# Kernel optimization log

Hardware: AMD Instinct MI355X
Metric: run time of the kernel (lower is better)

The kernel has to match this reference:

```python
import jax, jax.numpy as jnp
import numpy as np

H = 128; D = 16; L = 4
NP_ = 50000; NL_ = 10000; EPP = 500000; ELP = 100000; EPL = 100000


def _rbf(d):
    # GaussianSmearing(start=0, stop=8, num_gaussians=16)
    off = jnp.linspace(0.0, 8.0, D)
    coeff = -0.5 / ((8.0 / (D - 1)) ** 2)
    x = d[:, None] - off[None, :]
    return jnp.exp(coeff * x * x)


def _layer_norm(x, w, b, eps=1e-5):
    mu = jnp.mean(x, axis=-1, keepdims=True)
    var = jnp.var(x, axis=-1, keepdims=True)
    return (x - mu) * jax.lax.rsqrt(var + eps) * w + b


def _block(x_src, x_dst, src, dst, ea, Wf_, bf_, Ws_, bs_, bnw, bnb, lnw, lnb):
    # CGConv message: z = [x_i(dst), x_j(src), edge_attr]
    z = jnp.concatenate([x_dst[dst], x_src[src], ea], axis=-1)  # [E, 2H+D]
    m = jax.nn.sigmoid(z @ Wf_ + bf_) * jax.nn.softplus(z @ Ws_ + bs_)
    agg = jax.ops.segment_sum(m, dst, num_segments=x_dst.shape[0])
    # BatchNorm1d in eval mode with running_mean=0, running_var=1
    agg = agg * (bnw / jnp.sqrt(1.0 + 1e-5)) + bnb
    out = agg + x_dst            # CGConv internal residual
    out = _layer_norm(out, lnw, lnb)
    out = jax.nn.relu(out)
    return out + x_dst           # ResidualCGConvBlock residual (dropout=identity in eval)


def setup_inputs() -> dict:
    key = jax.random.key(0)
    ks = jax.random.split(key, 16)
    s = lambda n: 1.0 / np.sqrt(n)
    inp = {
        'x_protein': jax.random.normal(ks[0], (NP_, 6), jnp.float32),
        'x_ligand': jax.random.normal(ks[1], (NL_, 6), jnp.float32),
        'ei_pp': jnp.stack([jax.random.randint(ks[2], (EPP,), 0, NP_),
                            jax.random.randint(ks[3], (EPP,), 0, NP_)]).astype(jnp.int32),
        'ea_pp': jax.random.uniform(ks[4], (EPP,), jnp.float32, 0.0, 8.0),
        'ei_lp': jnp.stack([jax.random.randint(ks[5], (ELP,), 0, NL_),
                            jax.random.randint(ks[6], (ELP,), 0, NP_)]).astype(jnp.int32),
        'ea_lp': jax.random.uniform(ks[7], (ELP,), jnp.float32, 0.0, 8.0),
        'ei_pl': jnp.stack([jax.random.randint(ks[8], (EPL,), 0, NP_),
                            jax.random.randint(ks[9], (EPL,), 0, NL_)]).astype(jnp.int32),
        'ea_pl': jax.random.uniform(ks[10], (EPL,), jnp.float32, 0.0, 8.0),
        'Wp': jax.random.normal(ks[11], (6, H), jnp.float32) * s(6),
        'bp': jnp.zeros((H,), jnp.float32),
        'Wl': jax.random.normal(ks[12], (6, H), jnp.float32) * s(6),
        'bl': jnp.zeros((H,), jnp.float32),
        'Wf': jax.random.normal(ks[13], (L, 3, 2 * H + D, H), jnp.float32) * s(2 * H + D),
        'bf': jnp.zeros((L, 3, H), jnp.float32),
        'Ws': jax.random.normal(ks[14], (L, 3, 2 * H + D, H), jnp.float32) * s(2 * H + D),
        'bs': jnp.zeros((L, 3, H), jnp.float32),
        'bn_w': jnp.ones((L, 3, H), jnp.float32),
        'bn_b': jnp.zeros((L, 3, H), jnp.float32),
        'ln_w': jnp.ones((L, 3, H), jnp.float32),
        'ln_b': jnp.zeros((L, 3, H), jnp.float32),
        'lno_w': jnp.ones((H,), jnp.float32),
        'lno_b': jnp.zeros((H,), jnp.float32),
        'fc_w': jax.random.normal(ks[15], (H, 21), jnp.float32) * s(H),
        'fc_b': jnp.zeros((21,), jnp.float32),
    }
    return inp


def reference(x_protein, x_ligand, ei_pp, ea_pp, ei_lp, ea_lp, ei_pl, ea_pl,
              Wp, bp, Wl, bl, Wf, bf, Ws, bs, bn_w, bn_b, ln_w, ln_b,
              lno_w, lno_b, fc_w, fc_b):
    xp = x_protein @ Wp + bp
    xl = x_ligand @ Wl + bl
    rpp = _rbf(ea_pp); rlp = _rbf(ea_lp); rpl = _rbf(ea_pl)
    for l in range(L):
        # HeteroConv aggr='sum': protein receives from pp and lp; ligand from pl
        p_pp = _block(xp, xp, ei_pp[0], ei_pp[1], rpp, Wf[l, 0], bf[l, 0], Ws[l, 0], bs[l, 0],
                      bn_w[l, 0], bn_b[l, 0], ln_w[l, 0], ln_b[l, 0])
        p_lp = _block(xl, xp, ei_lp[0], ei_lp[1], rlp, Wf[l, 1], bf[l, 1], Ws[l, 1], bs[l, 1],
                      bn_w[l, 1], bn_b[l, 1], ln_w[l, 1], ln_b[l, 1])
        l_pl = _block(xp, xl, ei_pl[0], ei_pl[1], rpl, Wf[l, 2], bf[l, 2], Ws[l, 2], bs[l, 2],
                      bn_w[l, 2], bn_b[l, 2], ln_w[l, 2], ln_b[l, 2])
        xp, xl = p_pp + p_lp, l_pl
    out = _layer_norm(xp, lno_w, lno_b)
    return out @ fc_w + fc_b
```

## Files before the change

kernel.cpp:

```cpp
#include <hip/hip_runtime.h>
#include <hip/hip_bf16.h>
#include <math.h>

#define H 128
#define LOG2E 1.44269504f

typedef _Float16 f16;
typedef _Float16 f16x2 __attribute__((ext_vector_type(2)));
typedef _Float16 f16x8 __attribute__((ext_vector_type(8)));
typedef float f32x4 __attribute__((ext_vector_type(4)));
typedef float f32x2 __attribute__((ext_vector_type(2)));
typedef unsigned int uint32;

union u2h { uint32 u; f16x2 h; };
static __device__ __forceinline__ f16x2 as_h2(uint32 v){ u2h x; x.u = v; return x.h; }
static __device__ __forceinline__ uint32 pack_h2(float a, float b){
  u2h p; p.h = (f16x2){(f16)a, (f16)b}; return p.u;
}

static __device__ __forceinline__ int unperm64(int r){
  int base = r & ~63; int g = r & 63; int t = g >> 4; int j = g & 15;
  return base + 4*j + t;
}

#define NBIN 256
#define PREP_WP_N (4*1024*128)
#define PREP_WL_N (4*512*128)
#define RBF_N     (12*(NBIN+1)*128)

__global__ void prep_all(const float* __restrict__ Wf, const float* __restrict__ Ws,
                         const float* __restrict__ bfv, const float* __restrict__ bsv,
                         f16* __restrict__ Wt_p, float* __restrict__ Bias_p,
                         f16* __restrict__ Wt_l, float* __restrict__ Bias_l,
                         f16* __restrict__ T2,
                         const float* __restrict__ Xp, const float* __restrict__ Wp,
                         const float* __restrict__ bp, f16* __restrict__ Xph, int NP,
                         const float* __restrict__ Xl, const float* __restrict__ Wl,
                         const float* __restrict__ bl, f16* __restrict__ Xlh, int NL){
  int t = blockIdx.x*blockDim.x + threadIdx.x;
  if (t < PREP_WP_N){
    int k = t & 127; int idx = t >> 7;
    int rs = idx & 1023; int l = idx >> 10;
    int r = unperm64(rs);
    int rel, c, row0; const float* W; float bias = 0.f;
    if (r < 512){
      rel = (r < 256) ? 0 : 2;
      int rr = r & 255; int j = rr & 3;
      W = (j >= 2) ? Ws : Wf;
      c = ((rr >> 2) << 1) | (j & 1);
      row0 = 128;
    }
    else if (r < 640) { rel=0; c=r-512; row0=0; W=Wf; bias = bfv[(l*3+rel)*H+c]; }
    else if (r < 768) { rel=0; c=r-640; row0=0; W=Ws; bias = bsv[(l*3+rel)*H+c]; }
    else if (r < 896) { rel=1; c=r-768; row0=0; W=Wf; bias = bfv[(l*3+rel)*H+c]; }
    else              { rel=1; c=r-896; row0=0; W=Ws; bias = bsv[(l*3+rel)*H+c]; }
    Wt_p[t] = (f16)(LOG2E * W[((size_t)(l*3+rel)*272 + row0 + k)*H + c]);
    if (k == 0) Bias_p[l*1024 + r] = LOG2E * bias;
    return;
  }
  t -= PREP_WP_N;
  if (t < PREP_WL_N){
    int k = t & 127; int idx = t >> 7;
    int rs = idx & 511; int l = idx >> 9;
    int r = unperm64(rs);
    int rel, c, row0; const float* W; float bias = 0.f;
    if (r < 256){
      rel = 1; int j = r & 3;
      W = (j >= 2) ? Ws : Wf;
      c = ((r >> 2) << 1) | (j & 1);
      row0 = 128;
    }
    else if (r < 384) { rel=2; c=r-256; row0=0; W=Wf; bias = bfv[(l*3+rel)*H+c]; }
    else              { rel=2; c=r-384; row0=0; W=Ws; bias = bsv[(l*3+rel)*H+c]; }
    Wt_l[t] = (f16)(LOG2E * W[((size_t)(l*3+rel)*272 + row0 + k)*H + c]);
    if (k == 0) Bias_l[l*512 + r] = LOG2E * bias;
    return;
  }
  t -= PREP_WL_N;
  if (t < RBF_N){
    int c = t & 127;
    int b = (t >> 7) % (NBIN+1);
    int pr = t / ((NBIN+1)*128);
    float d0 = (float)b * (8.0f/(float)NBIN);
    const float* wf = Wf + ((size_t)pr*272 + 256)*H + c;
    const float* ws = Ws + ((size_t)pr*272 + 256)*H + c;
    float f0=0.f, s0=0.f;
    #pragma unroll
    for (int k=0;k<16;k++){
      float o = 0.533333333f*(float)k;
      float tt = d0 - o;
      float r0 = __expf(-1.7578125f*tt*tt);
      f0 += r0*wf[(size_t)k*H]; s0 += r0*ws[(size_t)k*H];
    }
    f16* o = T2 + ((size_t)(pr*(NBIN+1) + b))*256;
    int m = c >> 1, sub = c & 1;
    o[4*m + sub]     = (f16)(LOG2E * f0);
    o[4*m + 2 + sub] = (f16)(LOG2E * s0);
    return;
  }
  t -= RBF_N;
  {
    int idx = t;
    const float* Xin; const float* W; const float* b; f16* Xh;
    if (idx < NP*H){ Xin=Xp; W=Wp; b=bp; Xh=Xph; }
    else { idx -= NP*H; if (idx >= NL*H) return; Xin=Xl; W=Wl; b=bl; Xh=Xlh; }
    int n = idx >> 7, c = idx & 127;
    float acc = b[c];
    #pragma unroll
    for (int k=0;k<6;k++) acc += Xin[n*6+k] * W[k*H+c];
    Xh[idx] = (f16)acc;
  }
}

__global__ void hist3_k(const int* __restrict__ dpp, int Epp,
                        const int* __restrict__ dlp, int Elp,
                        const int* __restrict__ dpl, int Epl,
                        int* __restrict__ cpp, int* __restrict__ clp, int* __restrict__ cpl){
  int e = blockIdx.x*blockDim.x + threadIdx.x;
  if (e < Epp) atomicAdd(&cpp[dpp[e]], 1);
  else if (e < Epp+Elp) atomicAdd(&clp[dlp[e-Epp]], 1);
  else if (e < Epp+Elp+Epl) atomicAdd(&cpl[dpl[e-Epp-Elp]], 1);
}

#define SCH 1024

__global__ void __launch_bounds__(256) chunksum_k(
    const int* __restrict__ counts, int NP, int NL, int Cpp, int Cpl,
    int* __restrict__ chsum){
  __shared__ int wred[4];
  int b = blockIdx.x;
  const int* cnt; int n; int ch;
  if (b < Cpp){ cnt = counts; n = NP; ch = b; }
  else if (b < 2*Cpp){ cnt = counts + NP; n = NP; ch = b - Cpp; }
  else { cnt = counts + 2*NP; n = NL; ch = b - 2*Cpp; }
  int base = ch * SCH;
  int tid = threadIdx.x;
  int s = 0;
  #pragma unroll
  for (int j=0;j<SCH/256;j++){
    int i = base + tid + j*256;
    if (i < n) s += cnt[i];
  }
  #pragma unroll
  for (int o=32;o>=1;o>>=1) s += __shfl_xor(s,o,64);
  if ((tid & 63) == 0) wred[tid>>6] = s;
  __syncthreads();
  if (tid == 0) chsum[b] = wred[0]+wred[1]+wred[2]+wred[3];
}

__global__ void __launch_bounds__(192) scanmid_k(
    int* __restrict__ chsum, int Cpp, int Cpl, int NP, int NL,
    int* __restrict__ rp_pp, int* __restrict__ rp_lp, int* __restrict__ rp_pl){
  int wid = threadIdx.x >> 6, lane = threadIdx.x & 63;
  int C, off; int* rp_end; int n;
  if (wid == 0){ C = Cpp; off = 0;      rp_end = rp_pp; n = NP; }
  else if (wid == 1){ C = Cpp; off = Cpp; rp_end = rp_lp; n = NP; }
  else { C = Cpl; off = 2*Cpp; rp_end = rp_pl; n = NL; }
  int v = (lane < C) ? chsum[off + lane] : 0;
  int x = v;
  #pragma unroll
  for (int o=1;o<64;o<<=1){
    int y = __shfl_up(x, o, 64);
    if (lane >= o) x += y;
  }
  if (lane < C) chsum[off + lane] = x - v;
  if (lane == 63) rp_end[n] = x;
}

__global__ void __launch_bounds__(1024) scanfin_k(
    const int* __restrict__ counts, int NP, int NL, int Cpp, int Cpl,
    const int* __restrict__ chsum,
    int* __restrict__ rp_pp, int* __restrict__ cur_pp,
    int* __restrict__ rp_lp, int* __restrict__ cur_lp,
    int* __restrict__ rp_pl, int* __restrict__ cur_pl){
  __shared__ int wsum[16];
  int b = blockIdx.x;
  const int* cnt; int n, ch; int* rp; int* cur;
  if (b < Cpp){ cnt = counts; n = NP; ch = b; rp = rp_pp; cur = cur_pp; }
  else if (b < 2*Cpp){ cnt = counts + NP; n = NP; ch = b - Cpp; rp = rp_lp; cur = cur_lp; }
  else { cnt = counts + 2*NP; n = NL; ch = b - 2*Cpp; rp = rp_pl; cur = cur_pl; }
  int tid = threadIdx.x, lane = tid & 63, wid = tid >> 6;
  int i = ch*SCH + tid;
  int v = (i < n) ? cnt[i] : 0;
  int x = v;
  #pragma unroll
  for (int o=1;o<64;o<<=1){
    int y = __shfl_up(x, o, 64);
    if (lane >= o) x += y;
  }
  if (lane == 63) wsum[wid] = x;
  __syncthreads();
  if (wid == 0 && lane < 16){
    int w = wsum[lane];
    #pragma unroll
    for (int o=1;o<16;o<<=1){
      int y = __shfl_up(w, o, 64);
      if (lane >= o) w += y;
    }
    wsum[lane] = w;
  }
  __syncthreads();
  int waveoff = (wid == 0) ? 0 : wsum[wid-1];
  int ex = chsum[b] + waveoff + x - v;
  if (i < n){ rp[i] = ex; cur[i] = ex; }
}

__global__ void fill3_k(const int* __restrict__ ei_pp, const float* __restrict__ ea_pp, int Epp,
                        const int* __restrict__ ei_lp, const float* __restrict__ ea_lp, int Elp,
                        const int* __restrict__ ei_pl, const float* __restrict__ ea_pl, int Epl,
                        int* __restrict__ cur_pp, int2* __restrict__ e2_pp,
                        int* __restrict__ cur_lp, int2* __restrict__ e2_lp,
                        int* __restrict__ cur_pl, int2* __restrict__ e2_pl){
  int e = blockIdx.x*blockDim.x + threadIdx.x;
  if (e < Epp){
    int p = atomicAdd(&cur_pp[ei_pp[Epp + e]], 1);
    e2_pp[p] = make_int2(ei_pp[e], __float_as_int(ea_pp[e]));
  } else if (e < Epp+Elp){
    int i = e - Epp;
    int p = atomicAdd(&cur_lp[ei_lp[Elp + i]], 1);
    e2_lp[p] = make_int2(ei_lp[i], __float_as_int(ea_lp[i]));
  } else if (e < Epp+Elp+Epl){
    int i = e - Epp - Elp;
    int p = atomicAdd(&cur_pl[ei_pl[Epl + i]], 1);
    e2_pl[p] = make_int2(ei_pl[i], __float_as_int(ea_pl[i]));
  }
}

__global__ void __launch_bounds__(256) degbin_hist(
    const int* __restrict__ rp_pp, const int* __restrict__ rp_lp,
    const int* __restrict__ rp_pl, int NP, int NL, int* __restrict__ hist){
  __shared__ int lh[128];
  int t = threadIdx.x;
  if (t < 128) lh[t] = 0;
  __syncthreads();
  int i = blockIdx.x*256 + t;
  if (i < NP){
    int d = (rp_pp[i+1]-rp_pp[i]) + (rp_lp[i+1]-rp_lp[i]);
    if (d > 63) d = 63;
    atomicAdd(&lh[63 - d], 1);
  } else if (i < NP+NL){
    int n = i - NP;
    int d = rp_pl[n+1]-rp_pl[n];
    if (d > 63) d = 63;
    atomicAdd(&lh[64 + 63 - d], 1);
  }
  __syncthreads();
  if (t < 128 && lh[t]) atomicAdd(&hist[t], lh[t]);
}

__global__ void __launch_bounds__(128) degbin_scan(
    const int* __restrict__ hist, int* __restrict__ cursor){
  int t = threadIdx.x, lane = t & 63;
  int v = hist[t];
  int x = v;
  #pragma unroll
  for (int o=1;o<64;o<<=1){
    int y = __shfl_up(x, o, 64);
    if (lane >= o) x += y;
  }
  cursor[t] = x - v;
}

__global__ void __launch_bounds__(256) degbin_scatter(
    const int* __restrict__ rp_pp, const int* __restrict__ rp_lp,
    const int* __restrict__ rp_pl, int NP, int NL,
    int* __restrict__ cursor, int* __restrict__ perm){
  __shared__ int lh[128], lbase[128], lrank[128];
  int t = threadIdx.x;
  if (t < 128){ lh[t] = 0; lrank[t] = 0; }
  __syncthreads();
  int i = blockIdx.x*256 + t;
  int bin = -1, n = 0;
  if (i < NP){
    n = i;
    int d = (rp_pp[i+1]-rp_pp[i]) + (rp_lp[i+1]-rp_lp[i]);
    if (d > 63) d = 63;
    bin = 63 - d;
  } else if (i < NP+NL){
    n = i - NP;
    int d = rp_pl[n+1]-rp_pl[n];
    if (d > 63) d = 63;
    bin = 64 + 63 - d;
  }
  if (bin >= 0) atomicAdd(&lh[bin], 1);
  __syncthreads();
  if (t < 128 && lh[t]) lbase[t] = atomicAdd(&cursor[t], lh[t]);
  __syncthreads();
  if (bin >= 0){
    int r = atomicAdd(&lrank[bin], 1);
    perm[(bin < 64 ? 0 : NP) + lbase[bin] + r] = n;
  }
}

#define GR 8
__global__ void __launch_bounds__(256) gemm_tables(
    const f16* __restrict__ Xp, const f16* __restrict__ Wtp,
    const float* __restrict__ Biasp, f16* __restrict__ Outp,
    int strips_p, int tasks_p,
    const f16* __restrict__ Xl, const f16* __restrict__ Wtl,
    const float* __restrict__ Biasl, f16* __restrict__ Outl,
    int strips_l, int tasks_total){
  int wt = blockIdx.x*4 + (threadIdx.x >> 6);
  if (wt >= tasks_total) return;
  const f16 *X, *Wt; const float* Bias; f16* Out; int N, strips, g, chunk;
  if (wt < tasks_p){
    X=Xp; Wt=Wtp; Bias=Biasp; Out=Outp; N=1024; strips=strips_p;
    g = wt & 15; chunk = wt >> 4;
  } else {
    int w = wt - tasks_p;
    X=Xl; Wt=Wtl; Bias=Biasl; Out=Outl; N=512; strips=strips_l;
    g = w & 7; chunk = w >> 3;
  }
  int n0 = g << 6;
  int lane = threadIdx.x & 63;
  int lr = lane & 15, lq = lane >> 4;
  const f16x8* B0 = (const f16x8*)(const void*)(Wt + (size_t)(n0      + lr)*H);
  const f16x8* B1 = (const f16x8*)(const void*)(Wt + (size_t)(n0 + 16 + lr)*H);
  const f16x8* B2 = (const f16x8*)(const void*)(Wt + (size_t)(n0 + 32 + lr)*H);
  const f16x8* B3 = (const f16x8*)(const void*)(Wt + (size_t)(n0 + 48 + lr)*H);
  f16x8 b0_0=B0[lq], b0_1=B0[4+lq], b0_2=B0[8+lq], b0_3=B0[12+lq];
  f16x8 b1_0=B1[lq], b1_1=B1[4+lq], b1_2=B1[8+lq], b1_3=B1[12+lq];
  f16x8 b2_0=B2[lq], b2_1=B2[4+lq], b2_2=B2[8+lq], b2_3=B2[12+lq];
  f16x8 b3_0=B3[lq], b3_1=B3[4+lq], b3_2=B3[8+lq], b3_3=B3[12+lq];
  float4 bias = ((const float4*)(const void*)(Bias + n0))[lr];
  #pragma unroll 2
  for (int r=0;r<GR;r++){
    int strip = chunk*GR + r;
    if (strip >= strips) break;
    int m0 = strip << 4;
    const f16x8* A = (const f16x8*)(const void*)(X + (size_t)(m0+lr)*H);
    f16x8 a0 = A[lq], a1 = A[4+lq], a2 = A[8+lq], a3 = A[12+lq];
    f32x4 acc0 = {0.f,0.f,0.f,0.f}, acc1 = acc0, acc2 = acc0, acc3 = acc0;
    acc0 = __builtin_amdgcn_mfma_f32_16x16x32_f16(a0, b0_0, acc0, 0, 0, 0);
    acc1 = __builtin_amdgcn_mfma_f32_16x16x32_f16(a0, b1_0, acc1, 0, 0, 0);
    acc2 = __builtin_amdgcn_mfma_f32_16x16x32_f16(a0, b2_0, acc2, 0, 0, 0);
    acc3 = __builtin_amdgcn_mfma_f32_16x16x32_f16(a0, b3_0, acc3, 0, 0, 0);
    acc0 = __builtin_amdgcn_mfma_f32_16x16x32_f16(a1, b0_1, acc0, 0, 0, 0);
    acc1 = __builtin_amdgcn_mfma_f32_16x16x32_f16(a1, b1_1, acc1, 0, 0, 0);
    acc2 = __builtin_amdgcn_mfma_f32_16x16x32_f16(a1, b2_1, acc2, 0, 0, 0);
    acc3 = __builtin_amdgcn_mfma_f32_16x16x32_f16(a1, b3_1, acc3, 0, 0, 0);
    acc0 = __builtin_amdgcn_mfma_f32_16x16x32_f16(a2, b0_2, acc0, 0, 0, 0);
    acc1 = __builtin_amdgcn_mfma_f32_16x16x32_f16(a2, b1_2, acc1, 0, 0, 0);
    acc2 = __builtin_amdgcn_mfma_f32_16x16x32_f16(a2, b2_2, acc2, 0, 0, 0);
    acc3 = __builtin_amdgcn_mfma_f32_16x16x32_f16(a2, b3_2, acc3, 0, 0, 0);
    acc0 = __builtin_amdgcn_mfma_f32_16x16x32_f16(a3, b0_3, acc0, 0, 0, 0);
    acc1 = __builtin_amdgcn_mfma_f32_16x16x32_f16(a3, b1_3, acc1, 0, 0, 0);
    acc2 = __builtin_amdgcn_mfma_f32_16x16x32_f16(a3, b2_3, acc2, 0, 0, 0);
    acc3 = __builtin_amdgcn_mfma_f32_16x16x32_f16(a3, b3_3, acc3, 0, 0, 0);
    #pragma unroll
    for (int rr=0;rr<4;rr++){
      int row = m0 + lq*4 + rr;
      uint2 pk;
      pk.x = pack_h2(acc0[rr] + bias.x, acc1[rr] + bias.y);
      pk.y = pack_h2(acc2[rr] + bias.z, acc3[rr] + bias.w);
      *(uint2*)(void*)(Out + (size_t)row*N + n0 + 4*lr) = pk;
    }
  }
}

static __device__ __forceinline__ float act_msg(float F, float S){
  float sig = __builtin_amdgcn_rcpf(1.f + __builtin_amdgcn_exp2f(-F));
  float e   = __builtin_amdgcn_exp2f(fminf(S, 86.f));
  float sp  = 0.69314718f * __builtin_amdgcn_logf(1.f + e);
  return sig * sp;
}

#define BN_RSQ 0.9999950000374997f

static __device__ __forceinline__ void edge_nb(uint2 g, uint2 t,
                                               f16x2 fd2, f16x2 sd2, f32x2& acc){
  f16x2 F = (as_h2(g.x) + as_h2(t.x)) + fd2;
  f16x2 S = (as_h2(g.y) + as_h2(t.y)) + sd2;
  acc.x += act_msg((float)F.x, (float)S.x);
  acc.y += act_msg((float)F.y, (float)S.y);
}

static __device__ __forceinline__ void ln_stats_w(float v0, float v1, float& mu, float& var){
  float s = v0 + v1, q = v0*v0 + v1*v1;
  #pragma unroll
  for (int o=32;o>=1;o>>=1){ s += __shfl_xor(s,o,64); q += __shfl_xor(q,o,64); }
  mu = s * (1.f/128.f);
  var = q * (1.f/128.f) - mu*mu;
}

static __device__ __forceinline__ void aggregate(
    const int2* __restrict__ ev_arr, int e0, int e1,
    const uint2* __restrict__ G, int gstride, int goff,
    const uint2* __restrict__ Tb, int lane,
    f16x2 fd2, f16x2 sd2, f32x2& acc)
{
  for (int base = e0; base < e1; base += 64){
    int idx = base + lane;
    int2 ev = ev_arr[(idx < e1) ? idx : (e1-1)];
    float dd = __int_as_float(ev.y);
    int bnv = (int)__fmaf_rn(dd, (float)NBIN/8.0f, 0.5f);
    bnv = (bnv > NBIN) ? NBIN : bnv;
    int cnt = e1 - base; cnt = (cnt > 64) ? 64 : cnt;
    uint2 gA, tA, gB, tB, gC, tC;
    #define LDJ(gX, tX, j) { \
      int s_ = __builtin_amdgcn_readlane(ev.x, (j)); \
      int b_ = __builtin_amdgcn_readlane(bnv, (j)); \
      gX = G[(size_t)s_*gstride + goff + lane]; \
      tX = Tb[(size_t)b_*64 + lane]; }
    LDJ(gA, tA, 0);
    if (cnt > 1) LDJ(gB, tB, 1);
    if (cnt > 2) LDJ(gC, tC, 2);
    int j = 0;
    for (; j+5 < cnt; j += 3){
      edge_nb(gA, tA, fd2, sd2, acc); LDJ(gA, tA, j+3);
      edge_nb(gB, tB, fd2, sd2, acc); LDJ(gB, tB, j+4);
      edge_nb(gC, tC, fd2, sd2, acc); LDJ(gC, tC, j+5);
    }
    int rem = cnt - j;
    edge_nb(gA, tA, fd2, sd2, acc);
    if (rem > 3) LDJ(gA, tA, j+3);
    if (rem > 1) edge_nb(gB, tB, fd2, sd2, acc);
    if (rem > 4) LDJ(gB, tB, j+4);
    if (rem > 2) edge_nb(gC, tC, fd2, sd2, acc);
    if (rem > 3) edge_nb(gA, tA, fd2, sd2, acc);
    if (rem > 4) edge_nb(gB, tB, fd2, sd2, acc);
    #undef LDJ
  }
}

__global__ void __launch_bounds__(256) node_update(
    const f16* __restrict__ PT, const f16* __restrict__ LT,
    const f16* __restrict__ xp, const f16* __restrict__ xl,
    const int* __restrict__ pp_rp, const int2* __restrict__ pp_e2,
    const int* __restrict__ lp_rp, const int2* __restrict__ lp_e2,
    const int* __restrict__ pl_rp, const int2* __restrict__ pl_e2,
    const f16* __restrict__ T2,
    const float* __restrict__ bn_w, const float* __restrict__ bn_b,
    const float* __restrict__ ln_w, const float* __restrict__ ln_b,
    const int* __restrict__ perm,
    f16* __restrict__ xp_o, f16* __restrict__ xl_o,
    int layer, int NP, int NL, int PB)
{
  int wave = threadIdx.x >> 6;
  int lane = threadIdx.x & 63;
  const uint2* PTg = (const uint2*)(const void*)PT;
  if ((int)blockIdx.x < PB){
    int idx = blockIdx.x*4 + wave;
    if (idx >= NP) return;
    int node = perm[idx];
    f16x2 xh = as_h2(((const uint32*)(const void*)xp)[(size_t)node*64 + lane]);
    float xx = (float)xh.x, xy = (float)xh.y;
    const uint32* PTu = (const uint32*)(const void*)PT;
    const uint2*  LTg = (const uint2*)(const void*)LT;
    float o1_0, o1_1, o2_0, o2_1;
    {
      int pr = layer*3 + 0;
      f16x2 fd2 = as_h2(PTu[(size_t)node*512 + 256 + lane]);
      f16x2 sd2 = as_h2(PTu[(size_t)node*512 + 320 + lane]);
      const uint2* Tb = (const uint2*)(const void*)(T2 + (size_t)pr*(NBIN+1)*256);
      f32x2 acc = {0.f, 0.f};
      aggregate(pp_e2, pp_rp[node], pp_rp[node+1], PTg, 256, 0, Tb, lane, fd2, sd2, acc);
      float2 bw = ((const float2*)(const void*)(bn_w + pr*H))[lane];
      float2 bb = ((const float2*)(const void*)(bn_b + pr*H))[lane];
      float2 lw = ((const float2*)(const void*)(ln_w + pr*H))[lane];
      float2 lb = ((const float2*)(const void*)(ln_b + pr*H))[lane];
      float v0 = acc.x * (bw.x * BN_RSQ) + bb.x + xx;
      float v1 = acc.y * (bw.y * BN_RSQ) + bb.y + xy;
      float mu, var; ln_stats_w(v0, v1, mu, var);
      float rs = rsqrtf(var + 1e-5f);
      o1_0 = fmaxf((v0-mu)*rs*lw.x + lb.x, 0.f) + xx;
      o1_1 = fmaxf((v1-mu)*rs*lw.y + lb.y, 0.f) + xy;
    }
    {
      int pr = layer*3 + 1;
      f16x2 fd2 = as_h2(PTu[(size_t)node*512 + 384 + lane]);
      f16x2 sd2 = as_h2(PTu[(size_t)node*512 + 448 + lane]);
      const uint2* Tb = (const uint2*)(const void*)(T2 + (size_t)pr*(NBIN+1)*256);
      f32x2 acc = {0.f, 0.f};
      aggregate(lp_e2, lp_rp[node], lp_rp[node+1], LTg, 128, 0, Tb, lane, fd2, sd2, acc);
      float2 bw = ((const float2*)(const void*)(bn_w + pr*H))[lane];
      float2 bb = ((const float2*)(const void*)(bn_b + pr*H))[lane];
      float2 lw = ((const float2*)(const void*)(ln_w + pr*H))[lane];
      float2 lb = ((const float2*)(const void*)(ln_b + pr*H))[lane];
      float v0 = acc.x * (bw.x * BN_RSQ) + bb.x + xx;
      float v1 = acc.y * (bw.y * BN_RSQ) + bb.y + xy;
      float mu, var; ln_stats_w(v0, v1, mu, var);
      float rs = rsqrtf(var + 1e-5f);
      o2_0 = fmaxf((v0-mu)*rs*lw.x + lb.x, 0.f) + xx;
      o2_1 = fmaxf((v1-mu)*rs*lw.y + lb.y, 0.f) + xy;
    }
    float out0 = o1_0 + o2_0, out1 = o1_1 + o2_1;
    ((uint32*)(void*)xp_o)[(size_t)node*64 + lane] = pack_h2(out0, out1);
  } else {
    int idx = (blockIdx.x - PB)*4 + wave;
    if (idx >= NL) return;
    int node = perm[NP + idx];
    f16x2 xh = as_h2(((const uint32*)(const void*)xl)[(size_t)node*64 + lane]);
    float xx = (float)xh.x, xy = (float)xh.y;
    const uint32* LTu = (const uint32*)(const void*)LT;
    int pr = layer*3 + 2;
    f16x2 fd2 = as_h2(LTu[(size_t)node*256 + 128 + lane]);
    f16x2 sd2 = as_h2(LTu[(size_t)node*256 + 192 + lane]);
    const uint2* Tb = (const uint2*)(const void*)(T2 + (size_t)pr*(NBIN+1)*256);
    f32x2 acc = {0.f, 0.f};
    aggregate(pl_e2, pl_rp[node], pl_rp[node+1], PTg, 256, 64, Tb, lane, fd2, sd2, acc);
    float2 bw = ((const float2*)(const void*)(bn_w + pr*H))[lane];
    float2 bb = ((const float2*)(const void*)(bn_b + pr*H))[lane];
    float2 lw = ((const float2*)(const void*)(ln_w + pr*H))[lane];
    float2 lb = ((const float2*)(const void*)(ln_b + pr*H))[lane];
    float v0 = acc.x * (bw.x * BN_RSQ) + bb.x + xx;
    float v1 = acc.y * (bw.y * BN_RSQ) + bb.y + xy;
    float mu, var; ln_stats_w(v0, v1, mu, var);
    float rs = rsqrtf(var + 1e-5f);
    float out0 = fmaxf((v0-mu)*rs*lw.x + lb.x, 0.f) + xx;
    float out1 = fmaxf((v1-mu)*rs*lw.y + lb.y, 0.f) + xy;
    ((uint32*)(void*)xl_o)[(size_t)node*64 + lane] = pack_h2(out0, out1);
  }
}

__global__ void __launch_bounds__(128) final_k(const f16* __restrict__ xp,
    const float* __restrict__ lnw, const float* __restrict__ lnb,
    const float* __restrict__ fcw, const float* __restrict__ fcb,
    float* __restrict__ out, int N){
  __shared__ float sm[4];
  __shared__ float lnv[128];
  int node = blockIdx.x, c = threadIdx.x;
  float v = (float)xp[(size_t)node*H + c];
  float s = v, q = v*v;
  #pragma unroll
  for (int o=32;o>=1;o>>=1){ s += __shfl_xor(s,o,64); q += __shfl_xor(q,o,64); }
  __syncthreads();
  if ((c & 63) == 0){ sm[(c>>6)*2] = s; sm[(c>>6)*2+1] = q; }
  __syncthreads();
  float S = sm[0] + sm[2], Q = sm[1] + sm[3];
  float mu = S * (1.f/128.f);
  float var = Q * (1.f/128.f) - mu*mu;
  float ln = (v-mu)*rsqrtf(var+1e-5f)*lnw[c] + lnb[c];
  lnv[c] = ln;
  __syncthreads();
  if (c < 21){
    float a = fcb[c];
    #pragma unroll 4
    for (int i=0;i<128;i++) a += lnv[i]*fcw[i*21+c];
    out[(size_t)node*21 + c] = a;
  }
}

extern "C" void kernel_launch(void* const* d_in, const int* in_sizes, int n_in,
                              void* d_out, int out_size, void* d_ws, size_t ws_size,
                              hipStream_t stream){
  const float* x_protein = (const float*)d_in[0];
  const float* x_ligand  = (const float*)d_in[1];
  const int*   ei_pp = (const int*)d_in[2];
  const float* ea_pp = (const float*)d_in[3];
  const int*   ei_lp = (const int*)d_in[4];
  const float* ea_lp = (const float*)d_in[5];
  const int*   ei_pl = (const int*)d_in[6];
  const float* ea_pl = (const float*)d_in[7];
  const float* Wp  = (const float*)d_in[8];
  const float* bp  = (const float*)d_in[9];
  const float* Wl  = (const float*)d_in[10];
  const float* bl  = (const float*)d_in[11];
  const float* Wf  = (const float*)d_in[12];
  const float* bfv = (const float*)d_in[13];
  const float* Wsv = (const float*)d_in[14];
  const float* bsv = (const float*)d_in[15];
  const float* bn_w = (const float*)d_in[16];
  const float* bn_b = (const float*)d_in[17];
  const float* ln_w = (const float*)d_in[18];
  const float* ln_b = (const float*)d_in[19];
  const float* lno_w = (const float*)d_in[20];
  const float* lno_b = (const float*)d_in[21];
  const float* fc_w = (const float*)d_in[22];
  const float* fc_b = (const float*)d_in[23];

  int NP  = in_sizes[0]/6, NL = in_sizes[1]/6;
  int EPP = in_sizes[3], ELP = in_sizes[5], EPL = in_sizes[7];

  char* ws = (char*)d_ws;
  size_t off = 0;
  auto alloc = [&](size_t bytes)->void*{
    void* p = ws + off; off = (off + bytes + 255) & ~(size_t)255; return p;
  };

  f16* xpA = (f16*)alloc((size_t)NP*H*2);
  f16* xpB = (f16*)alloc((size_t)NP*H*2);
  f16* xlA = (f16*)alloc((size_t)NL*H*2);
  f16* xlB = (f16*)alloc((size_t)NL*H*2);
  f16* PT    = (f16*)alloc((size_t)NP*1024*2);
  f16* LT    = (f16*)alloc((size_t)NL*512*2);
  f16* Wt_p  = (f16*)alloc((size_t)4*1024*H*2);
  f16* Wt_l  = (f16*)alloc((size_t)4*512*H*2);
  float* Bias_p = (float*)alloc((size_t)4*1024*4);
  float* Bias_l = (float*)alloc((size_t)4*512*4);
  f16* T2    = (f16*)alloc((size_t)12*(NBIN+1)*256*2);
  int* counts = (int*)alloc((size_t)(2*NP+NL)*4);
  int* rp_pp  = (int*)alloc((size_t)(NP+1)*4);
  int* cur_pp = (int*)alloc((size_t)NP*4);
  int* rp_lp  = (int*)alloc((size_t)(NP+1)*4);
  int* cur_lp = (int*)alloc((size_t)NP*4);
  int* rp_pl  = (int*)alloc((size_t)(NL+1)*4);
  int* cur_pl = (int*)alloc((size_t)NL*4);
  int2* e2_pp = (int2*)alloc((size_t)EPP*8);
  int2* e2_lp = (int2*)alloc((size_t)ELP*8);
  int2* e2_pl = (int2*)alloc((size_t)EPL*8);
  int Cpp = (NP + SCH - 1) / SCH;
  int Cpl = (NL + SCH - 1) / SCH;
  int* chsum = (int*)alloc((size_t)(2*Cpp + Cpl)*4);
  int* dhist  = (int*)alloc(128*4);
  int* dcur   = (int*)alloc(128*4);
  int* perm   = (int*)alloc((size_t)(NP+NL)*4);
  (void)ws_size; (void)n_in; (void)out_size;

  size_t prep_total = (size_t)PREP_WP_N + PREP_WL_N + RBF_N + (size_t)(NP+NL)*H;
  prep_all<<<(prep_total+255)/256, 256, 0, stream>>>(Wf, Wsv, bfv, bsv,
      Wt_p, Bias_p, Wt_l, Bias_l, T2,
      x_protein, Wp, bp, xpA, NP,
      x_ligand,  Wl, bl, xlA, NL);
  hipMemsetAsync(counts, 0, (size_t)(2*NP+NL)*4, stream);
  hipMemsetAsync(dhist, 0, 128*4, stream);
  int* cnt_pp = counts; int* cnt_lp = counts + NP; int* cnt_pl = counts + 2*NP;
  int Etot = EPP + ELP + EPL;
  hist3_k<<<(Etot+255)/256, 256, 0, stream>>>(ei_pp+EPP, EPP, ei_lp+ELP, ELP, ei_pl+EPL, EPL,
                                              cnt_pp, cnt_lp, cnt_pl);
  chunksum_k<<<2*Cpp + Cpl, 256, 0, stream>>>(counts, NP, NL, Cpp, Cpl, chsum);
  scanmid_k<<<1, 192, 0, stream>>>(chsum, Cpp, Cpl, NP, NL, rp_pp, rp_lp, rp_pl);
  scanfin_k<<<2*Cpp + Cpl, 1024, 0, stream>>>(counts, NP, NL, Cpp, Cpl, chsum,
                                              rp_pp, cur_pp, rp_lp, cur_lp, rp_pl, cur_pl);
  fill3_k<<<(Etot+255)/256, 256, 0, stream>>>(ei_pp, ea_pp, EPP, ei_lp, ea_lp, ELP,
                                              ei_pl, ea_pl, EPL,
                                              cur_pp, e2_pp, cur_lp, e2_lp, cur_pl, e2_pl);
  int nbks = (NP + NL + 255) / 256;
  degbin_hist<<<nbks, 256, 0, stream>>>(rp_pp, rp_lp, rp_pl, NP, NL, dhist);
  degbin_scan<<<1, 128, 0, stream>>>(dhist, dcur);
  degbin_scatter<<<nbks, 256, 0, stream>>>(rp_pp, rp_lp, rp_pl, NP, NL, dcur, perm);

  f16* xp_cur = xpA; f16* xp_nxt = xpB;
  f16* xl_cur = xlA; f16* xl_nxt = xlB;
  int strips_p = NP >> 4, strips_l = NL >> 4;
  int tasks_p = 16 * ((strips_p + GR - 1) / GR);
  int tasks_l = 8  * ((strips_l + GR - 1) / GR);
  int tasks_total = tasks_p + tasks_l;
  int PB = (NP + 3) / 4, LB = (NL + 3) / 4;
  for (int l=0; l<4; l++){
    gemm_tables<<<(tasks_total+3)/4, 256, 0, stream>>>(
        xp_cur, Wt_p + (size_t)l*1024*H, Bias_p + l*1024, PT, strips_p, tasks_p,
        xl_cur, Wt_l + (size_t)l*512*H,  Bias_l + l*512,  LT, strips_l, tasks_total);
    node_update<<<PB + LB, 256, 0, stream>>>(PT, LT, xp_cur, xl_cur,
        rp_pp, e2_pp, rp_lp, e2_lp, rp_pl, e2_pl, T2,
        bn_w, bn_b, ln_w, ln_b, perm, xp_nxt, xl_nxt, l, NP, NL, PB);
    f16* t;
    t = xp_cur; xp_cur = xp_nxt; xp_nxt = t;
    t = xl_cur; xl_cur = xl_nxt; xl_nxt = t;
  }

  final_k<<<NP, 128, 0, stream>>>(xp_cur, lno_w, lno_b, fc_w, fc_b, (float*)d_out, NP);
}
```

Baseline: 751.8 us.

## Compute final layernorm and FC projection with MFMA in split-f16 precision

Replaces the per-node final kernel, which used one 128-thread block per node with shared-memory reductions and a scalar 21-column dot product, with a wave-per-16-node MFMA kernel. The FC weights are pre-split into high and low f16 parts during prep, and the normalized activations are split likewise. Three MFMA products (hi*hi, lo*hi, hi*lo) are summed to stay close to fp32 accuracy. This removes syncthreads and launch overhead for 50k blocks, at the cost of extra prep work and padding 21 output columns up to 32.

After: 685.2 us. -8.9%, faster.

```diff
diff --git a/kernel.cpp b/kernel.cpp
--- a/kernel.cpp
+++ b/kernel.cpp
@@ -27,12 +27,15 @@
 #define PREP_WP_N (4*1024*128)
 #define PREP_WL_N (4*512*128)
 #define RBF_N     (12*(NBIN+1)*128)
+#define FC_N      (32*128)
 
 __global__ void prep_all(const float* __restrict__ Wf, const float* __restrict__ Ws,
                          const float* __restrict__ bfv, const float* __restrict__ bsv,
                          f16* __restrict__ Wt_p, float* __restrict__ Bias_p,
                          f16* __restrict__ Wt_l, float* __restrict__ Bias_l,
                          f16* __restrict__ T2,
+                         const float* __restrict__ fcw,
+                         f16* __restrict__ fwhi, f16* __restrict__ fwlo,
                          const float* __restrict__ Xp, const float* __restrict__ Wp,
                          const float* __restrict__ bp, f16* __restrict__ Xph, int NP,
                          const float* __restrict__ Xl, const float* __restrict__ Wl,
@@ -99,6 +102,15 @@
     return;
   }
   t -= RBF_N;
+  if (t < FC_N){
+    int col = t >> 7, k = t & 127;
+    float w = (col < 21) ? fcw[k*21 + col] : 0.f;
+    f16 hi = (f16)w;
+    fwhi[col*128 + k] = hi;
+    fwlo[col*128 + k] = (f16)(w - (float)hi);
+    return;
+  }
+  t -= FC_N;
   {
     int idx = t;
     const float* Xin; const float* W; const float* b; f16* Xh;
@@ -513,31 +525,76 @@
   }
 }
 
-__global__ void __launch_bounds__(128) final_k(const f16* __restrict__ xp,
+__global__ void __launch_bounds__(256) final_k(const f16* __restrict__ xp,
     const float* __restrict__ lnw, const float* __restrict__ lnb,
-    const float* __restrict__ fcw, const float* __restrict__ fcb,
-    float* __restrict__ out, int N){
-  __shared__ float sm[4];
-  __shared__ float lnv[128];
-  int node = blockIdx.x, c = threadIdx.x;
-  float v = (float)xp[(size_t)node*H + c];
-  float s = v, q = v*v;
-  #pragma unroll
-  for (int o=32;o>=1;o>>=1){ s += __shfl_xor(s,o,64); q += __shfl_xor(q,o,64); }
-  __syncthreads();
-  if ((c & 63) == 0){ sm[(c>>6)*2] = s; sm[(c>>6)*2+1] = q; }
-  __syncthreads();
-  float S = sm[0] + sm[2], Q = sm[1] + sm[3];
-  float mu = S * (1.f/128.f);
-  float var = Q * (1.f/128.f) - mu*mu;
-  float ln = (v-mu)*rsqrtf(var+1e-5f)*lnw[c] + lnb[c];
-  lnv[c] = ln;
-  __syncthreads();
-  if (c < 21){
-    float a = fcb[c];
-    #pragma unroll 4
-    for (int i=0;i<128;i++) a += lnv[i]*fcw[i*21+c];
-    out[(size_t)node*21 + c] = a;
+    const f16* __restrict__ fwhi, const f16* __restrict__ fwlo,
+    const float* __restrict__ fcb, float* __restrict__ out, int N){
+  int wave = threadIdx.x >> 6, lane = threadIdx.x & 63;
+  int m0 = (blockIdx.x*4 + wave) << 4;
+  if (m0 >= N) return;
+  int lr = lane & 15, lq = lane >> 4;
+  int node = m0 + lr; if (node >= N) node = N - 1;
+  const f16x8* X = (const f16x8*)(const void*)(xp + (size_t)node*H);
+  f16x8 x0 = X[lq], x1 = X[4+lq], x2 = X[8+lq], x3 = X[12+lq];
+  float s = 0.f, q = 0.f;
+  #pragma unroll
+  for (int i=0;i<8;i++){
+    float a=(float)x0[i], b=(float)x1[i], c=(float)x2[i], d=(float)x3[i];
+    s += a+b+c+d; q += a*a+b*b+c*c+d*d;
+  }
+  s += __shfl_xor(s,16,64); q += __shfl_xor(q,16,64);
+  s += __shfl_xor(s,32,64); q += __shfl_xor(q,32,64);
+  float mu = s*(1.f/128.f), var = q*(1.f/128.f) - mu*mu;
+  float rs = rsqrtf(var + 1e-5f);
+  f16x8 xs0 = x0, xs1 = x1, xs2 = x2, xs3 = x3;
+  f16x8 ah[4], al[4];
+  const float4* LW = (const float4*)(const void*)lnw;
+  const float4* LB = (const float4*)(const void*)lnb;
+  #define MKFRAG(F, XS) { \
+    int b4 = F*8 + lq*2; \
+    float4 w0 = LW[b4], w1 = LW[b4+1]; \
+    float4 c0 = LB[b4], c1 = LB[b4+1]; \
+    float l0=((float)XS[0]-mu)*rs*w0.x + c0.x; \
+    float l1=((float)XS[1]-mu)*rs*w0.y + c0.y; \
+    float l2=((float)XS[2]-mu)*rs*w0.z + c0.z; \
+    float l3=((float)XS[3]-mu)*rs*w0.w + c0.w; \
+    float l4=((float)XS[4]-mu)*rs*w1.x + c1.x; \
+    float l5=((float)XS[5]-mu)*rs*w1.y + c1.y; \
+    float l6=((float)XS[6]-mu)*rs*w1.z + c1.z; \
+    float l7=((float)XS[7]-mu)*rs*w1.w + c1.w; \
+    f16x8 hh = {(f16)l0,(f16)l1,(f16)l2,(f16)l3,(f16)l4,(f16)l5,(f16)l6,(f16)l7}; \
+    f16x8 ll = {(f16)(l0-(float)hh[0]),(f16)(l1-(float)hh[1]), \
+                (f16)(l2-(float)hh[2]),(f16)(l3-(float)hh[3]), \
+                (f16)(l4-(float)hh[4]),(f16)(l5-(float)hh[5]), \
+                (f16)(l6-(float)hh[6]),(f16)(l7-(float)hh[7])}; \
+    ah[F] = hh; al[F] = ll; }
+  MKFRAG(0, xs0); MKFRAG(1, xs1); MKFRAG(2, xs2); MKFRAG(3, xs3);
+  #undef MKFRAG
+  const f16x8* BH0 = (const f16x8*)(const void*)(fwhi + (size_t)lr*128);
+  const f16x8* BH1 = (const f16x8*)(const void*)(fwhi + (size_t)(16+lr)*128);
+  const f16x8* BL0 = (const f16x8*)(const void*)(fwlo + (size_t)lr*128);
+  const f16x8* BL1 = (const f16x8*)(const void*)(fwlo + (size_t)(16+lr)*128);
+  f32x4 acc0 = {0.f,0.f,0.f,0.f}, acc1 = acc0;
+  #pragma unroll
+  for (int f=0; f<4; f++){
+    f16x8 bh0 = BH0[f*4+lq], bh1 = BH1[f*4+lq];
+    f16x8 bl0 = BL0[f*4+lq], bl1 = BL1[f*4+lq];
+    acc0 = __builtin_amdgcn_mfma_f32_16x16x32_f16(ah[f], bh0, acc0, 0, 0, 0);
+    acc1 = __builtin_amdgcn_mfma_f32_16x16x32_f16(ah[f], bh1, acc1, 0, 0, 0);
+    acc0 = __builtin_amdgcn_mfma_f32_16x16x32_f16(al[f], bh0, acc0, 0, 0, 0);
+    acc1 = __builtin_amdgcn_mfma_f32_16x16x32_f16(al[f], bh1, acc1, 0, 0, 0);
+    acc0 = __builtin_amdgcn_mfma_f32_16x16x32_f16(ah[f], bl0, acc0, 0, 0, 0);
+    acc1 = __builtin_amdgcn_mfma_f32_16x16x32_f16(ah[f], bl1, acc1, 0, 0, 0);
+  }
+  float bias0 = fcb[lr];
+  float bias1 = (lr < 5) ? fcb[16 + lr] : 0.f;
+  #pragma unroll
+  for (int rr=0; rr<4; rr++){
+    int row = m0 + lq*4 + rr;
+    if (row < N){
+      out[(size_t)row*21 + lr] = acc0[rr] + bias0;
+      if (lr < 5) out[(size_t)row*21 + 16 + lr] = acc1[rr] + bias1;
+    }
   }
 }
 
@@ -589,6 +646,8 @@
   float* Bias_p = (float*)alloc((size_t)4*1024*4);
   float* Bias_l = (float*)alloc((size_t)4*512*4);
   f16* T2    = (f16*)alloc((size_t)12*(NBIN+1)*256*2);
+  f16* fwhi  = (f16*)alloc((size_t)32*128*2);
+  f16* fwlo  = (f16*)alloc((size_t)32*128*2);
   int* counts = (int*)alloc((size_t)(2*NP+NL)*4);
   int* rp_pp  = (int*)alloc((size_t)(NP+1)*4);
   int* cur_pp = (int*)alloc((size_t)NP*4);
@@ -607,9 +666,10 @@
   int* perm   = (int*)alloc((size_t)(NP+NL)*4);
   (void)ws_size; (void)n_in; (void)out_size;
 
-  size_t prep_total = (size_t)PREP_WP_N + PREP_WL_N + RBF_N + (size_t)(NP+NL)*H;
+  size_t prep_total = (size_t)PREP_WP_N + PREP_WL_N + RBF_N + FC_N + (size_t)(NP+NL)*H;
   prep_all<<<(prep_total+255)/256, 256, 0, stream>>>(Wf, Wsv, bfv, bsv,
       Wt_p, Bias_p, Wt_l, Bias_l, T2,
+      fc_w, fwhi, fwlo,
       x_protein, Wp, bp, xpA, NP,
       x_ligand,  Wl, bl, xlA, NL);
   hipMemsetAsync(counts, 0, (size_t)(2*NP+NL)*4, stream);
@@ -649,5 +709,7 @@
     t = xl_cur; xl_cur = xl_nxt; xl_nxt = t;
   }
 
-  final_k<<<NP, 128, 0, stream>>>(xp_cur, lno_w, lno_b, fc_w, fc_b, (float*)d_out, NP);
-}
+  int fstrips = (NP + 15) >> 4;
+  final_k<<<(fstrips+3)/4, 256, 0, stream>>>(xp_cur, lno_w, lno_b,
+      fwhi, fwlo, fc_b, (float*)d_out, NP);
+}
```
